# Kernel tuning notes

Measured on AMD Instinct MI355X. Metric: run time of the kernel, lower is better.

Reference implementation:

```python
import jax, jax.numpy as jnp
import numpy as np

T = 5          # Newton-Schulz iterations
EPS = 1e-05


def reference(X):
    # X: (B, C, L); training-mode IterNorm whitening with num_groups=1
    B, C, L = X.shape
    x = jnp.transpose(X, (1, 0, 2)).reshape(C, -1)        # (d, m)
    d, m = x.shape
    mean = jnp.mean(x, axis=-1, keepdims=True)
    xc = x - mean                                         # (d, m)
    I = jnp.eye(d, dtype=X.dtype)
    Sigma = I * EPS + (xc @ xc.T) * (1.0 / m)             # (d, d)
    rTr = 1.0 / jnp.trace(Sigma)                          # scalar
    Sigma_N = Sigma * rTr
    P = I
    for _ in range(T):
        P = 1.5 * P - 0.5 * (P @ P @ P) @ Sigma_N
    wm = P * jnp.sqrt(rTr)                                # whitening matrix
    xn = wm @ xc                                          # (d, m)
    Xn = jnp.transpose(xn.reshape(C, B, L), (1, 0, 2))
    return Xn


def setup_inputs() -> dict:
    key = jax.random.key(0)
    X = jax.random.normal(key, (32, 64, 8192), dtype=jnp.float32)
    return {"X": X}
```

## Files before the change

kernel.cpp:

```cpp
#include <hip/hip_runtime.h>
#include <math.h>

#define L_DIM   8192
#define NCH     64
#define M_TOT_F 262144.0f
#define EPS_F   1e-5f

typedef float f32x4 __attribute__((ext_vector_type(4)));
typedef short bf16x8 __attribute__((ext_vector_type(8)));

union U8 { unsigned u[4]; bf16x8 v; };

__device__ __forceinline__ void cvt2(float f0, float f1, unsigned& h, unsigned& l) {
    unsigned u0 = __float_as_uint(f0), u1 = __float_as_uint(f1);
    h = (u0 >> 16) | (u1 & 0xFFFF0000u);
    float r0 = f0 - __uint_as_float(u0 & 0xFFFF0000u);
    float r1 = f1 - __uint_as_float(u1 & 0xFFFF0000u);
    l = (__float_as_uint(r0) >> 16) | (__float_as_uint(r1) & 0xFFFF0000u);
}

__device__ __forceinline__ void split16(float v, unsigned short& h, unsigned short& l) {
    unsigned u = __float_as_uint(v);
    h = (unsigned short)(u >> 16);
    float r = v - __uint_as_float(u & 0xFFFF0000u);
    l = (unsigned short)(__float_as_uint(r) >> 16);
}

__device__ __forceinline__ f32x4 mfma16(bf16x8 a, bf16x8 b, f32x4 c) {
    return __builtin_amdgcn_mfma_f32_16x16x32_bf16(a, b, c, 0, 0, 0);
}

__device__ __forceinline__ f32x4 fzero() {
    f32x4 z; z[0] = 0.f; z[1] = 0.f; z[2] = 0.f; z[3] = 0.f; return z;
}

#define GTPB 4
__global__ __launch_bounds__(256) void gram_kernel(const float* __restrict__ X,
                                                   float* __restrict__ P) {
    __shared__ __align__(16) unsigned short hplane[2][64 * 72];
    __shared__ __align__(16) unsigned short lplane[2][64 * 72];
    const int tid  = threadIdx.x;
    const int w    = tid >> 6;
    const int lane = tid & 63;
    const int m    = lane & 15;
    const int q    = lane >> 4;
    const int lrow = tid >> 2;
    const int lq16 = (tid & 3) << 4;

    f32x4 acc1[4], acc2[4];
#pragma unroll
    for (int nb = 0; nb < 4; ++nb) { acc1[nb] = fzero(); acc2[nb] = fzero(); }
    float sacc = 0.f;

    const int tile0 = blockIdx.x * GTPB;
    float4 v[4];
    {
        int t = tile0;
        const float* src = X + ((size_t)((t >> 7) * NCH + lrow)) * L_DIM + ((t & 127) << 6) + lq16;
#pragma unroll
        for (int i = 0; i < 4; ++i) v[i] = ((const float4*)src)[i];
    }

    for (int t = 0; t < GTPB; ++t) {
        const int p = t & 1;
#pragma unroll
        for (int i = 0; i < 4; ++i) sacc += v[i].x + v[i].y + v[i].z + v[i].w;
#pragma unroll
        for (int i = 0; i < 4; ++i) {
            unsigned h0, l0, h1, l1;
            cvt2(v[i].x, v[i].y, h0, l0);
            cvt2(v[i].z, v[i].w, h1, l1);
            uint2 hh; hh.x = h0; hh.y = h1;
            uint2 ll; ll.x = l0; ll.y = l1;
            *(uint2*)&hplane[p][lrow * 72 + lq16 + 4 * i] = hh;
            *(uint2*)&lplane[p][lrow * 72 + lq16 + 4 * i] = ll;
        }
        if (t + 1 < GTPB) {
            int tn = tile0 + t + 1;
            const float* src = X + ((size_t)((tn >> 7) * NCH + lrow)) * L_DIM + ((tn & 127) << 6) + lq16;
#pragma unroll
            for (int i = 0; i < 4; ++i) v[i] = ((const float4*)src)[i];
        }
        __syncthreads();
#pragma unroll
        for (int k0 = 0; k0 < 64; k0 += 32) {
            bf16x8 a = *(const bf16x8*)&hplane[p][(16 * w + m) * 72 + k0 + 8 * q];
#pragma unroll
            for (int nb = 0; nb < 4; ++nb) {
                bf16x8 bh = *(const bf16x8*)&hplane[p][(16 * nb + m) * 72 + k0 + 8 * q];
                bf16x8 bl = *(const bf16x8*)&lplane[p][(16 * nb + m) * 72 + k0 + 8 * q];
                acc1[nb] = mfma16(a, bh, acc1[nb]);
                acc2[nb] = mfma16(a, bl, acc2[nb]);
            }
        }
    }

    float* base = P + (size_t)blockIdx.x * 8256;
#pragma unroll
    for (int nb = 0; nb < 4; ++nb)
#pragma unroll
        for (int r = 0; r < 4; ++r) {
            int grow = 16 * w + 4 * q + r;
            int gcol = 16 * nb + m;
            base[grow * 64 + gcol]        = acc1[nb][r];
            base[4096 + grow * 64 + gcol] = acc2[nb][r];
        }
    sacc += __shfl_xor(sacc, 1);
    sacc += __shfl_xor(sacc, 2);
    if ((tid & 3) == 0) base[8192 + lrow] = sacc;
}

__global__ __launch_bounds__(256) void reduce_kernel(const float* __restrict__ P,
                                                     float* __restrict__ ws) {
    const int tid = threadIdx.x;
    const int w = tid >> 6, lane = tid & 63;
    const int e0 = blockIdx.x * 64;
    float a = 0.f;
#pragma unroll 8
    for (int i = 0; i < 256; ++i)
        a += P[(size_t)(w * 256 + i) * 8256 + e0 + lane];
    __shared__ float red[4][64];
    red[w][lane] = a;
    __syncthreads();
    if (w == 0)
        ws[e0 + lane] = red[0][lane] + red[1][lane] + red[2][lane] + red[3][lane];
}

__device__ __forceinline__ void mm_core(f32x4* acc,
                                        const unsigned short* __restrict__ Xh,
                                        const unsigned short* __restrict__ Xl,
                                        const unsigned short* __restrict__ Yh,
                                        const unsigned short* __restrict__ Yl,
                                        int w, int m, int q) {
#pragma unroll
    for (int k0 = 0; k0 < 64; k0 += 32) {
        bf16x8 xh = *(const bf16x8*)&Xh[(16 * w + m) * 72 + k0 + 8 * q];
        bf16x8 xl = *(const bf16x8*)&Xl[(16 * w + m) * 72 + k0 + 8 * q];
#pragma unroll
        for (int nb = 0; nb < 4; ++nb) {
            bf16x8 yh = *(const bf16x8*)&Yh[(16 * nb + m) * 72 + k0 + 8 * q];
            bf16x8 yl = *(const bf16x8*)&Yl[(16 * nb + m) * 72 + k0 + 8 * q];
            acc[nb] = mfma16(xh, yh, acc[nb]);
            acc[nb] = mfma16(xh, yl, acc[nb]);
            acc[nb] = mfma16(xl, yh, acc[nb]);
        }
    }
}

__device__ __forceinline__ void mm_pl(unsigned short* __restrict__ Dh,
                                      unsigned short* __restrict__ Dl,
                                      const unsigned short* __restrict__ Xh,
                                      const unsigned short* __restrict__ Xl,
                                      const unsigned short* __restrict__ Yh,
                                      const unsigned short* __restrict__ Yl,
                                      int w, int m, int q) {
    f32x4 acc[4];
#pragma unroll
    for (int nb = 0; nb < 4; ++nb) acc[nb] = fzero();
    mm_core(acc, Xh, Xl, Yh, Yl, w, m, q);
#pragma unroll
    for (int nb = 0; nb < 4; ++nb)
#pragma unroll
        for (int r = 0; r < 4; ++r) {
            int row = 16 * w + 4 * q + r, col = 16 * nb + m;
            unsigned short h, l;
            split16(acc[nb][r], h, l);
            Dh[row * 72 + col] = h;
            Dl[row * 72 + col] = l;
        }
}

__global__ __launch_bounds__(256) void ns_kernel(float* __restrict__ ws) {
    __shared__ __align__(16) float Pf[64 * 68];
    __shared__ __align__(16) unsigned short Ph[64 * 72], Pl[64 * 72];
    __shared__ __align__(16) unsigned short Sh[64 * 72], Sl[64 * 72];
    __shared__ __align__(16) unsigned short T1h[64 * 72], T1l[64 * 72];
    __shared__ __align__(16) unsigned short T2h[64 * 72], T2l[64 * 72];
    __shared__ float mu[64];
    __shared__ float scal[2];

    const int tid = threadIdx.x;
    const int w = tid >> 6, lane = tid & 63;
    const int m = lane & 15, q = lane >> 4;
    const float inv_m = 1.0f / M_TOT_F;

    if (tid < 64) mu[tid] = ws[8192 + tid] * inv_m;
    __syncthreads();

    for (int e = tid; e < 4096; e += 256) {
        int i = e >> 6, j = e & 63;
        float g = (ws[e] + ws[4096 + e] + ws[4096 + (j << 6) + i]) * inv_m;
        Pf[i * 68 + j] = g - mu[i] * mu[j] + ((i == j) ? EPS_F : 0.f);
    }
    __syncthreads();

    if (tid < 64) {
        float v = Pf[tid * 68 + tid];
#pragma unroll
        for (int off = 32; off >= 1; off >>= 1) v += __shfl_xor(v, off);
        if (tid == 0) { scal[0] = 1.0f / v; scal[1] = sqrtf(1.0f / v); }
    }
    __syncthreads();
    const float rTr = scal[0];

    for (int e = tid; e < 4096; e += 256) {
        int i = e >> 6, j = e & 63;
        float sn = Pf[i * 68 + j] * rTr;
        unsigned short h, l;
        split16(sn, h, l);
        Sh[i * 72 + j] = h; Sl[i * 72 + j] = l;
        float pv = ((i == j) ? 1.5f : 0.f) - 0.5f * sn;
        Pf[i * 68 + j] = pv;
        split16(pv, h, l);
        Ph[i * 72 + j] = h; Pl[i * 72 + j] = l;
    }
    __syncthreads();

    for (int it = 0; it < 4; ++it) {
        mm_pl(T1h, T1l, Ph, Pl, Ph, Pl, w, m, q);
        __syncthreads();
        mm_pl(T2h, T2l, T1h, T1l, Ph, Pl, w, m, q);
        __syncthreads();
        f32x4 acc[4];
#pragma unroll
        for (int nb = 0; nb < 4; ++nb) acc[nb] = fzero();
        mm_core(acc, T2h, T2l, Sh, Sl, w, m, q);
#pragma unroll
        for (int nb = 0; nb < 4; ++nb)
#pragma unroll
            for (int r = 0; r < 4; ++r) {
                int row = 16 * w + 4 * q + r, col = 16 * nb + m;
                int idx = row * 68 + col;
                float pv = 1.5f * Pf[idx] - 0.5f * acc[nb][r];
                Pf[idx] = pv;
                unsigned short h, l;
                split16(pv, h, l);
                Ph[row * 72 + col] = h;
                Pl[row * 72 + col] = l;
            }
        __syncthreads();
    }

    const float s = scal[1];
    unsigned short* hp = (unsigned short*)ws;
    unsigned short* lp = hp + 4096;
    for (int e = tid; e < 4096; e += 256) {
        int i = e >> 6, j = e & 63;
        float v = Pf[i * 68 + j] * s;
        unsigned short h, l;
        split16(v, h, l);
        hp[e] = h;
        lp[e] = l;
    }
    if (tid < 64) {
        float a = 0.f;
#pragma unroll 8
        for (int k = 0; k < 64; ++k) a += Pf[tid * 68 + k] * mu[k];
        ws[8256 + tid] = -a * s;
    }
}

#define ATPB 4
__global__ __launch_bounds__(256) void apply_kernel(const float* __restrict__ X,
                                                    float* __restrict__ Y,
                                                    const float* __restrict__ ws) {
    __shared__ __align__(16) unsigned short hplane[2][4096];
    __shared__ __align__(16) unsigned short lplane[2][4096];
    const int tid  = threadIdx.x;
    const int w    = tid >> 6;
    const int lane = tid & 63;
    const int m    = lane & 15;
    const int q    = lane >> 4;
    const int cp   = tid & 31;
    const int lg   = tid >> 5;

    const unsigned short* hp = (const unsigned short*)ws;
    const unsigned short* lp = hp + 4096;
    bf16x8 Ah[2], Al[2];
#pragma unroll
    for (int kk = 0; kk < 2; ++kk) {
        Ah[kk] = *(const bf16x8*)&hp[(16 * w + m) * 64 + 32 * kk + 8 * q];
        Al[kk] = *(const bf16x8*)&lp[(16 * w + m) * 64 + 32 * kk + 8 * q];
    }
    const float4 bias4 = *(const float4*)&ws[8256 + 16 * w + 4 * q];

    float4 va[2], vb[2];
    {
        int tile = blockIdx.x * ATPB;
        const float* xb = X + (size_t)(tile >> 7) * (NCH * L_DIM) + ((tile & 127) << 6)
                          + (size_t)(2 * cp) * L_DIM + 4 * lg;
#pragma unroll
        for (int s = 0; s < 2; ++s) {
            va[s] = *(const float4*)(xb + 32 * s);
            vb[s] = *(const float4*)(xb + 32 * s + L_DIM);
        }
    }

    for (int t = 0; t < ATPB; ++t) {
        int tile = blockIdx.x * ATPB + t;
        int bidx = tile >> 7;
        int l0   = (tile & 127) << 6;
        const int p = t & 1;
        unsigned* hw = (unsigned*)hplane[p];
        unsigned* lw = (unsigned*)lplane[p];

#pragma unroll
        for (int s = 0; s < 2; ++s) {
            float fa[4], fb[4];
            *(float4*)fa = va[s];
            *(float4*)fb = vb[s];
#pragma unroll
            for (int i = 0; i < 4; ++i) {
                int l = 4 * lg + 32 * s + i;
                unsigned h, lo2;
                cvt2(fa[i], fb[i], h, lo2);
                int widx = l * 32 + (((cp >> 2) ^ (l & 7)) << 2) + (cp & 3);
                hw[widx] = h;
                lw[widx] = lo2;
            }
        }

        if (t + 1 < ATPB) {
            int tn = tile + 1;
            const float* xb = X + (size_t)(tn >> 7) * (NCH * L_DIM) + ((tn & 127) << 6)
                              + (size_t)(2 * cp) * L_DIM + 4 * lg;
#pragma unroll
            for (int s = 0; s < 2; ++s) {
                va[s] = *(const float4*)(xb + 32 * s);
                vb[s] = *(const float4*)(xb + 32 * s + L_DIM);
            }
        }
        __syncthreads();

        f32x4 acc[4];
#pragma unroll
        for (int nb = 0; nb < 4; ++nb) {
            acc[nb][0] = bias4.x; acc[nb][1] = bias4.y;
            acc[nb][2] = bias4.z; acc[nb][3] = bias4.w;
        }
#pragma unroll
        for (int kk = 0; kk < 2; ++kk)
#pragma unroll
            for (int nb = 0; nb < 4; ++nb) {
                int l = 16 * nb + m;
                int saddr = l * 64 + ((((4 * kk + q) ^ (l & 7))) << 3);
                bf16x8 bh = *(const bf16x8*)&hplane[p][saddr];
                bf16x8 bl = *(const bf16x8*)&lplane[p][saddr];
                acc[nb] = mfma16(Ah[kk], bh, acc[nb]);
                acc[nb] = mfma16(Ah[kk], bl, acc[nb]);
                acc[nb] = mfma16(Al[kk], bh, acc[nb]);
            }

#pragma unroll
        for (int nb = 0; nb < 4; ++nb)
#pragma unroll
            for (int rr = 0; rr < 4; ++rr)
                Y[((size_t)bidx * NCH + 16 * w + 4 * q + rr) * L_DIM + l0 + 16 * nb + m] = acc[nb][rr];
    }
}

extern "C" void kernel_launch(void* const* d_in, const int* in_sizes, int n_in,
                              void* d_out, int out_size, void* d_ws, size_t ws_size,
                              hipStream_t stream) {
    const float* X = (const float*)d_in[0];
    float* Y  = (float*)d_out;
    float* ws = (float*)d_ws;
    float* scratch = (float*)d_out;

    hipLaunchKernelGGL(gram_kernel,   dim3(1024), dim3(256), 0, stream, X, scratch);
    hipLaunchKernelGGL(reduce_kernel, dim3(129),  dim3(256), 0, stream, scratch, ws);
    hipLaunchKernelGGL(ns_kernel,     dim3(1),    dim3(256), 0, stream, ws);
    hipLaunchKernelGGL(apply_kernel,  dim3(1024), dim3(256), 0, stream, X, Y, ws);
}
```

Before: 156.3 us.

## Load gram tiles directly in MFMA fragment layout and split reduce accumulators

The gram kernel now has each lane load the exact row and k-slice it needs as an MFMA A-operand. It keeps the A fragments in registers and writes bf16 hi/lo planes to shared memory in a fragment-ordered, conflict-free layout instead of a padded row-major one. This removes the shared-memory reload of the A operand and changes the global load pattern to two 32-byte chunks per lane. The reduce kernel uses four independent accumulators to break the serial add dependency chain, which slightly reorders the floating-point summation.

```diff
diff --git a/kernel.cpp b/kernel.cpp
--- a/kernel.cpp
+++ b/kernel.cpp
@@ -37,15 +37,14 @@
 #define GTPB 4
 __global__ __launch_bounds__(256) void gram_kernel(const float* __restrict__ X,
                                                    float* __restrict__ P) {
-    __shared__ __align__(16) unsigned short hplane[2][64 * 72];
-    __shared__ __align__(16) unsigned short lplane[2][64 * 72];
+    __shared__ __align__(16) unsigned short hfrag[2][4096];
+    __shared__ __align__(16) unsigned short lfrag[2][4096];
     const int tid  = threadIdx.x;
     const int w    = tid >> 6;
     const int lane = tid & 63;
     const int m    = lane & 15;
     const int q    = lane >> 4;
-    const int lrow = tid >> 2;
-    const int lq16 = (tid & 3) << 4;
+    const int row  = 16 * w + m;
 
     f32x4 acc1[4], acc2[4];
 #pragma unroll
@@ -56,43 +55,52 @@
     float4 v[4];
     {
         int t = tile0;
-        const float* src = X + ((size_t)((t >> 7) * NCH + lrow)) * L_DIM + ((t & 127) << 6) + lq16;
-#pragma unroll
-        for (int i = 0; i < 4; ++i) v[i] = ((const float4*)src)[i];
+        const float* src = X + ((size_t)((t >> 7) * NCH + row)) * L_DIM + ((t & 127) << 6) + 8 * q;
+        v[0] = *(const float4*)(src);
+        v[1] = *(const float4*)(src + 4);
+        v[2] = *(const float4*)(src + 32);
+        v[3] = *(const float4*)(src + 36);
     }
 
     for (int t = 0; t < GTPB; ++t) {
         const int p = t & 1;
 #pragma unroll
         for (int i = 0; i < 4; ++i) sacc += v[i].x + v[i].y + v[i].z + v[i].w;
-#pragma unroll
-        for (int i = 0; i < 4; ++i) {
-            unsigned h0, l0, h1, l1;
-            cvt2(v[i].x, v[i].y, h0, l0);
-            cvt2(v[i].z, v[i].w, h1, l1);
-            uint2 hh; hh.x = h0; hh.y = h1;
-            uint2 ll; ll.x = l0; ll.y = l1;
-            *(uint2*)&hplane[p][lrow * 72 + lq16 + 4 * i] = hh;
-            *(uint2*)&lplane[p][lrow * 72 + lq16 + 4 * i] = ll;
-        }
+
+        bf16x8 Ah[2], Al[2];
+#pragma unroll
+        for (int k = 0; k < 2; ++k) {
+            U8 H, L;
+            cvt2(v[2 * k].x,     v[2 * k].y,     H.u[0], L.u[0]);
+            cvt2(v[2 * k].z,     v[2 * k].w,     H.u[1], L.u[1]);
+            cvt2(v[2 * k + 1].x, v[2 * k + 1].y, H.u[2], L.u[2]);
+            cvt2(v[2 * k + 1].z, v[2 * k + 1].w, H.u[3], L.u[3]);
+            Ah[k] = H.v; Al[k] = L.v;
+            int chunk = ((w * 2 + k) * 4 + q) * 16 + m;
+            *(bf16x8*)&hfrag[p][chunk * 8] = H.v;
+            *(bf16x8*)&lfrag[p][chunk * 8] = L.v;
+        }
+
         if (t + 1 < GTPB) {
             int tn = tile0 + t + 1;
-            const float* src = X + ((size_t)((tn >> 7) * NCH + lrow)) * L_DIM + ((tn & 127) << 6) + lq16;
-#pragma unroll
-            for (int i = 0; i < 4; ++i) v[i] = ((const float4*)src)[i];
-        }
-        __syncthreads();
-#pragma unroll
-        for (int k0 = 0; k0 < 64; k0 += 32) {
-            bf16x8 a = *(const bf16x8*)&hplane[p][(16 * w + m) * 72 + k0 + 8 * q];
+            const float* src = X + ((size_t)((tn >> 7) * NCH + row)) * L_DIM + ((tn & 127) << 6) + 8 * q;
+            v[0] = *(const float4*)(src);
+            v[1] = *(const float4*)(src + 4);
+            v[2] = *(const float4*)(src + 32);
+            v[3] = *(const float4*)(src + 36);
+        }
+        __syncthreads();
+
+#pragma unroll
+        for (int k = 0; k < 2; ++k)
 #pragma unroll
             for (int nb = 0; nb < 4; ++nb) {
-                bf16x8 bh = *(const bf16x8*)&hplane[p][(16 * nb + m) * 72 + k0 + 8 * q];
-                bf16x8 bl = *(const bf16x8*)&lplane[p][(16 * nb + m) * 72 + k0 + 8 * q];
-                acc1[nb] = mfma16(a, bh, acc1[nb]);
-                acc2[nb] = mfma16(a, bl, acc2[nb]);
-            }
-        }
+                int chunk = ((nb * 2 + k) * 4 + q) * 16 + m;
+                bf16x8 bh = *(const bf16x8*)&hfrag[p][chunk * 8];
+                bf16x8 bl = *(const bf16x8*)&lfrag[p][chunk * 8];
+                acc1[nb] = mfma16(Ah[k], bh, acc1[nb]);
+                acc2[nb] = mfma16(Ah[k], bl, acc2[nb]);
+            }
     }
 
     float* base = P + (size_t)blockIdx.x * 8256;
@@ -105,9 +113,9 @@
             base[grow * 64 + gcol]        = acc1[nb][r];
             base[4096 + grow * 64 + gcol] = acc2[nb][r];
         }
-    sacc += __shfl_xor(sacc, 1);
-    sacc += __shfl_xor(sacc, 2);
-    if ((tid & 3) == 0) base[8192 + lrow] = sacc;
+    sacc += __shfl_xor(sacc, 16);
+    sacc += __shfl_xor(sacc, 32);
+    if (q == 0) base[8192 + 16 * w + m] = sacc;
 }
 
 __global__ __launch_bounds__(256) void reduce_kernel(const float* __restrict__ P,
@@ -115,10 +123,16 @@
     const int tid = threadIdx.x;
     const int w = tid >> 6, lane = tid & 63;
     const int e0 = blockIdx.x * 64;
-    float a = 0.f;
+    float a0 = 0.f, a1 = 0.f, a2 = 0.f, a3 = 0.f;
 #pragma unroll 8
-    for (int i = 0; i < 256; ++i)
-        a += P[(size_t)(w * 256 + i) * 8256 + e0 + lane];
+    for (int i = 0; i < 64; ++i) {
+        const float* p = P + (size_t)(w * 256 + 4 * i) * 8256 + e0 + lane;
+        a0 += p[0];
+        a1 += p[8256];
+        a2 += p[2 * 8256];
+        a3 += p[3 * 8256];
+    }
+    float a = (a0 + a1) + (a2 + a3);
     __shared__ float red[4][64];
     red[w][lane] = a;
     __syncthreads();
```

Measured after the change: 157.2 us. No clear change (+0.6%).
